# Optimization experiments

Hardware: AMD Instinct MI355X
Metric: run time of the kernel (lower is better)

## Reference

```python
import jax, jax.numpy as jnp
import numpy as np

EPSILON = 0.01
NITER = 5
EPS_MASS = 1e-9
EPS_LSE = 1e-6


def setup_inputs() -> dict:
    key = jax.random.key(0)
    k1, k2 = jax.random.split(key)
    y = jax.random.uniform(k1, (16, 1, 48, 48), dtype=jnp.float32)
    y_target = jax.random.uniform(k2, (16, 1, 48, 48), dtype=jnp.float32)
    return {"y": y, "y_target": y_target}


def _grid_points(h, w):
    # torch.linspace(0, h-1, h)/h == arange(h)/h
    yg = jnp.arange(h, dtype=jnp.float32) / h
    xg = jnp.arange(w, dtype=jnp.float32) / w
    gy, gx = jnp.meshgrid(yg, xg, indexing="ij")
    return jnp.stack([gy.reshape(-1), gx.reshape(-1)], axis=-1)  # [n, 2]


def reference(y, y_target):
    b, c, h, w = y_target.shape
    g = _grid_points(h, w)                     # [n, 2], same for x and y measures
    # cost_matrix with p=2: sum_k |g_i - g_j|^2 ; grids identical across batch,
    # so compute once as [n, n] and broadcast.
    C = ((g[:, None, :] - g[None, :, :]) ** 2).sum(-1)  # [n, n]

    mass_x = jnp.clip(y.reshape(b, -1), 0.0, 1e9) + EPS_MASS
    mass_y = jnp.clip(y_target.reshape(b, -1), 0.0, 1e9) + EPS_MASS
    mu = mass_x / mass_x.sum(-1, keepdims=True)   # [b, n]
    nu = mass_y / mass_y.sum(-1, keepdims=True)   # [b, n]
    log_mu = jnp.log(mu)
    log_nu = jnp.log(nu)

    def M(u, v):
        # (-C_ij + u_i + v_j) / epsilon, shape [b, n, n]
        return (-C[None, :, :] + u[:, :, None] + v[:, None, :]) / EPSILON

    def lse(A):
        # faithful to original: log(sum(exp(A), axis=2) + 1e-6) (non-shifted)
        return jnp.log(jnp.exp(A).sum(2) + EPS_LSE)

    u = jnp.zeros_like(mu)
    v = jnp.zeros_like(nu)
    for _ in range(NITER):
        u = EPSILON * (log_mu - lse(M(u, v))) + u
        v = EPSILON * (log_nu - lse(jnp.swapaxes(M(u, v), 1, 2))) + v

    pi = jnp.exp(M(u, v))                      # [b, n, n] transport plan
    cost = (pi * C[None, :, :]).sum((1, 2))    # [b]
    return jnp.mean(cost)
```

## Files before the change

kernel.cpp:

```cpp
#include <hip/hip_runtime.h>


#define TPB 576
#define STRIDE 72

typedef __attribute__((ext_vector_type(8))) short short8;
typedef __attribute__((ext_vector_type(4))) short short4v;
typedef __attribute__((ext_vector_type(4))) float f32x4;

__device__ __forceinline__ void splitb(float x, short& hi, short& lo) {
    union { float f; unsigned u; } a, h, l;
    a.f = x;
    h.u = a.u & 0xffff0000u;
    hi  = (short)(h.u >> 16);
    l.f = x - h.f;
    lo  = (short)(l.u >> 16);
}

__device__ __forceinline__ f32x4 mm16(short8 a, short8 b, f32x4 c) {
    return __builtin_amdgcn_mfma_f32_16x16x32_bf16(a, b, c, 0, 0, 0);
}

__device__ __forceinline__ f32x4 tile3(const short* Ah, const short* Al,
                                       const short* Bh, const short* Bl,
                                       int aOff, int bOff, f32x4 acc)
{
    short8 ah0 = *(const short8*)(Ah + aOff);
    short8 ah1 = *(const short8*)(Ah + aOff + 32);
    short8 al0 = *(const short8*)(Al + aOff);
    short8 al1 = *(const short8*)(Al + aOff + 32);
    short8 bh0 = *(const short8*)(Bh + bOff);
    short8 bh1 = *(const short8*)(Bh + bOff + 32);
    short8 bl0 = *(const short8*)(Bl + bOff);
    short8 bl1 = *(const short8*)(Bl + bOff + 32);
    f32x4 x = acc;
    f32x4 y = {0.f, 0.f, 0.f, 0.f};
    x = mm16(ah0, bh0, x);
    y = mm16(ah1, bh1, y);
    x = mm16(ah0, bl0, x);
    y = mm16(ah1, bl1, y);
    x = mm16(al0, bh0, x);
    y = mm16(al1, bh1, y);
    return x + y;
}

__global__ __launch_bounds__(TPB) void sinkhorn_kernel(const float* __restrict__ y,
                                                       const float* __restrict__ yt,
                                                       float* __restrict__ out)
{
    __shared__ __align__(16) short sThi[48*STRIDE],  sTlo[48*STRIDE];
    __shared__ __align__(16) short sTDhi[48*STRIDE], sTDlo[48*STRIDE];
    __shared__ __align__(16) short sWhi[48*STRIDE],  sWlo[48*STRIDE];
    __shared__ __align__(16) short sPhi[48*STRIDE],  sPlo[48*STRIDE];
    __shared__ __align__(16) float sS[2304];
    __shared__ float red[32];

    const int t    = threadIdx.x;
    const int b    = blockIdx.x;
    const int lane = t & 63;
    const int wid  = t >> 6;
    const int tr   = wid / 3;
    const int tc   = wid - tr * 3;
    const int n15  = lane & 15;
    const int quad = lane >> 4;
    const int kq   = quad * 8;
    const int aOff   = (tr * 16 + n15) * STRIDE + kq;
    const int bOff   = (tc * 16 + n15) * STRIDE + kq;
    const int prBase = tr * 16 + quad * 4;
    const int pn     = tc * 16 + n15;
    const int wOffB  = (t / 12) * STRIDE + (t % 12) * 4;

    const float EPS = 0.01f, RINV = 100.0f;

    for (int i = t; i < 48 * STRIDE; i += TPB) {
        sWhi[i] = 0; sWlo[i] = 0; sPhi[i] = 0; sPlo[i] = 0;
        int a  = i / STRIDE;
        int bb = i - a * STRIDE;
        short th = 0, tl = 0, dh = 0, dl = 0;
        if (bb < 48) {
            float d   = (float)a / 48.0f - (float)bb / 48.0f;
            float dsq = d * d;
            float e   = __expf(-dsq * RINV);
            splitb(e, th, tl);
            splitb(e * dsq, dh, dl);
        }
        sThi[i] = th; sTlo[i] = tl; sTDhi[i] = dh; sTDlo[i] = dl;
    }

    const f32x4 y4  = ((const f32x4*)(y  + b * 2304))[t];
    const f32x4 yt4 = ((const f32x4*)(yt + b * 2304))[t];
    float mx[4], my[4];
#pragma unroll
    for (int c = 0; c < 4; ++c) {
        mx[c] = fminf(fmaxf(y4[c],  0.f), 1e9f) + 1e-9f;
        my[c] = fminf(fmaxf(yt4[c], 0.f), 1e9f) + 1e-9f;
    }
    float sx = mx[0] + mx[1] + mx[2] + mx[3];
    float sy = my[0] + my[1] + my[2] + my[3];
#pragma unroll
    for (int off = 32; off > 0; off >>= 1) {
        sx += __shfl_down(sx, off);
        sy += __shfl_down(sy, off);
    }
    if (lane == 0) { red[wid] = sx; red[16 + wid] = sy; }
    __syncthreads();
    if (t == 0) {
        float ax = 0.f, ay = 0.f;
#pragma unroll
        for (int w = 0; w < TPB / 64; ++w) { ax += red[w]; ay += red[16 + w]; }
        red[0] = ax; red[16] = ay;
    }
    __syncthreads();
    const float rsx = 1.0f / red[0], rsy = 1.0f / red[16];

    float lmu_[4], lnu_[4];
#pragma unroll
    for (int c = 0; c < 4; ++c) {
        lmu_[c] = __logf(mx[c] * rsx);
        lnu_[c] = __logf(my[c] * rsy);
    }

    float u_[4]  = {0, 0, 0, 0}, v_[4]  = {0, 0, 0, 0};
    float wu_[4] = {1, 1, 1, 1}, wv_[4] = {1, 1, 1, 1};

    {
        short4v oneh = {(short)0x3F80, (short)0x3F80, (short)0x3F80, (short)0x3F80};
        short4v zer  = {0, 0, 0, 0};
        *(short4v*)(sWhi + wOffB) = oneh;
        *(short4v*)(sWlo + wOffB) = zer;
    }
    __syncthreads();

    const f32x4 zz = {0.f, 0.f, 0.f, 0.f};

    auto do_upd = [&](float (&ab)[4], const float (&lm)[4], float (&wc)[4],
                      const f32x4& S4) {
        short4v h4, l4;
#pragma unroll
        for (int c = 0; c < 4; ++c) {
            float lse = __logf(wc[c] * S4[c] + 1e-6f);
            ab[c] = EPS * (lm[c] - lse) + ab[c];
            wc[c] = __expf(RINV * ab[c]);
            short hh, ll; splitb(wc[c], hh, ll);
            h4[c] = hh; l4[c] = ll;
        }
        *(short4v*)(sWhi + wOffB) = h4;
        *(short4v*)(sWlo + wOffB) = l4;
    };

    for (int half = 0; half < 10; ++half) {
        f32x4 p = tile3(sThi, sTlo, sWhi, sWlo, aOff, bOff, zz);
#pragma unroll
        for (int rg = 0; rg < 4; ++rg) {
            short h, l; splitb(p[rg], h, l);
            int o = (prBase + rg) * STRIDE + pn;
            sPhi[o] = h; sPlo[o] = l;
        }
        __syncthreads();
        f32x4 s = tile3(sThi, sTlo, sPhi, sPlo, aOff, bOff, zz);
#pragma unroll
        for (int rg = 0; rg < 4; ++rg)
            sS[(prBase + rg) * 48 + pn] = s[rg];
        __syncthreads();
        f32x4 S4 = *(const f32x4*)(sS + 4 * t);
        if ((half & 1) == 0) do_upd(u_, lmu_, wu_, S4);
        else                 do_upd(v_, lnu_, wv_, S4);
        __syncthreads();
    }

    f32x4 p1 = tile3(sThi, sTlo, sWhi, sWlo, aOff, bOff, zz);
    f32x4 p2 = tile3(sTDhi, sTDlo, sWhi, sWlo, aOff, bOff, zz);
#pragma unroll
    for (int rg = 0; rg < 4; ++rg) {
        short h, l; splitb(p1[rg], h, l);
        int o = (prBase + rg) * STRIDE + pn;
        sPhi[o] = h; sPlo[o] = l;
    }
    __syncthreads();
    f32x4 sacc = tile3(sTDhi, sTDlo, sPhi, sPlo, aOff, bOff, zz);
    __syncthreads();
#pragma unroll
    for (int rg = 0; rg < 4; ++rg) {
        short h, l; splitb(p2[rg], h, l);
        int o = (prBase + rg) * STRIDE + pn;
        sPhi[o] = h; sPlo[o] = l;
    }
    __syncthreads();
    sacc = tile3(sThi, sTlo, sPhi, sPlo, aOff, bOff, sacc);
#pragma unroll
    for (int rg = 0; rg < 4; ++rg)
        sS[(prBase + rg) * 48 + pn] = sacc[rg];
    __syncthreads();

    f32x4 S4 = *(const f32x4*)(sS + 4 * t);
    float local = wu_[0] * S4[0] + wu_[1] * S4[1] + wu_[2] * S4[2] + wu_[3] * S4[3];
#pragma unroll
    for (int off = 32; off > 0; off >>= 1) local += __shfl_down(local, off);
    if (lane == 0) red[wid] = local;
    __syncthreads();
    if (t == 0) {
        float c = 0.f;
#pragma unroll
        for (int w = 0; w < TPB / 64; ++w) c += red[w];
        atomicAdd(out, c * (1.0f / 16.0f));
    }
}

extern "C" void kernel_launch(void* const* d_in, const int* in_sizes, int n_in,
                              void* d_out, int out_size, void* d_ws, size_t ws_size,
                              hipStream_t stream)
{
    (void)in_sizes; (void)n_in; (void)d_ws; (void)ws_size; (void)out_size;
    const float* y  = (const float*)d_in[0];
    const float* yt = (const float*)d_in[1];
    float* out = (float*)d_out;

    hipMemsetAsync(out, 0, sizeof(float), stream);
    sinkhorn_kernel<<<16, TPB, 0, stream>>>(y, yt, out);
}
```

Baseline: 73.26 us.

## Keep kernel tiles in registers, use multiplicative scaling updates with single-bf16 operands

The Gaussian kernel factors now live in registers instead of LDS. The u/v log-domain updates become direct multiplicative scaling-vector updates, which removes the log and exp per element. The B operands (W, P) switch from a hi/lo bf16 split to a single round-to-nearest bf16, cutting the MFMAs per tile from 6 to 4. It also removes one barrier per half-iteration and the sS staging buffer, and replaces the memset plus atomic with a per-block partial sum and a second small reduction kernel. In exchange, the lower-precision operands risk accuracy, and the extra launch adds overhead.

```diff
diff --git a/kernel.cpp b/kernel.cpp
--- a/kernel.cpp
+++ b/kernel.cpp
@@ -5,54 +5,36 @@
 #define STRIDE 72
 
 typedef __attribute__((ext_vector_type(8))) short short8;
-typedef __attribute__((ext_vector_type(4))) short short4v;
 typedef __attribute__((ext_vector_type(4))) float f32x4;
 
 __device__ __forceinline__ void splitb(float x, short& hi, short& lo) {
-    union { float f; unsigned u; } a, h, l;
+    union { float f; unsigned u; } a, h;
     a.f = x;
     h.u = a.u & 0xffff0000u;
     hi  = (short)(h.u >> 16);
+    union { float f; unsigned u; } l;
     l.f = x - h.f;
     lo  = (short)(l.u >> 16);
 }
 
+__device__ __forceinline__ short bf16rne(float x) {
+    union { float f; unsigned u; } a;
+    a.f = x;
+    unsigned r = a.u + 0x7fffu + ((a.u >> 16) & 1u);
+    return (short)(r >> 16);
+}
+
 __device__ __forceinline__ f32x4 mm16(short8 a, short8 b, f32x4 c) {
     return __builtin_amdgcn_mfma_f32_16x16x32_bf16(a, b, c, 0, 0, 0);
 }
 
-__device__ __forceinline__ f32x4 tile3(const short* Ah, const short* Al,
-                                       const short* Bh, const short* Bl,
-                                       int aOff, int bOff, f32x4 acc)
-{
-    short8 ah0 = *(const short8*)(Ah + aOff);
-    short8 ah1 = *(const short8*)(Ah + aOff + 32);
-    short8 al0 = *(const short8*)(Al + aOff);
-    short8 al1 = *(const short8*)(Al + aOff + 32);
-    short8 bh0 = *(const short8*)(Bh + bOff);
-    short8 bh1 = *(const short8*)(Bh + bOff + 32);
-    short8 bl0 = *(const short8*)(Bl + bOff);
-    short8 bl1 = *(const short8*)(Bl + bOff + 32);
-    f32x4 x = acc;
-    f32x4 y = {0.f, 0.f, 0.f, 0.f};
-    x = mm16(ah0, bh0, x);
-    y = mm16(ah1, bh1, y);
-    x = mm16(ah0, bl0, x);
-    y = mm16(ah1, bl1, y);
-    x = mm16(al0, bh0, x);
-    y = mm16(al1, bh1, y);
-    return x + y;
-}
-
 __global__ __launch_bounds__(TPB) void sinkhorn_kernel(const float* __restrict__ y,
                                                        const float* __restrict__ yt,
-                                                       float* __restrict__ out)
+                                                       float* __restrict__ partials)
 {
-    __shared__ __align__(16) short sThi[48*STRIDE],  sTlo[48*STRIDE];
-    __shared__ __align__(16) short sTDhi[48*STRIDE], sTDlo[48*STRIDE];
-    __shared__ __align__(16) short sWhi[48*STRIDE],  sWlo[48*STRIDE];
-    __shared__ __align__(16) short sPhi[48*STRIDE],  sPlo[48*STRIDE];
-    __shared__ __align__(16) float sS[2304];
+    __shared__ __align__(16) short sW[48 * STRIDE];
+    __shared__ __align__(16) short sP[48 * STRIDE];
+    __shared__ __align__(16) short sP2[48 * STRIDE];
     __shared__ float red[32];
 
     const int t    = threadIdx.x;
@@ -64,36 +46,50 @@
     const int n15  = lane & 15;
     const int quad = lane >> 4;
     const int kq   = quad * 8;
-    const int aOff   = (tr * 16 + n15) * STRIDE + kq;
-    const int bOff   = (tc * 16 + n15) * STRIDE + kq;
+    const int aRow = tr * 16 + n15;
+    const int bBase = (tc * 16 + n15) * STRIDE;
     const int prBase = tr * 16 + quad * 4;
     const int pn     = tc * 16 + n15;
-    const int wOffB  = (t / 12) * STRIDE + (t % 12) * 4;
-
-    const float EPS = 0.01f, RINV = 100.0f;
+    const int wAddr  = prBase * STRIDE + pn;
+
+    short8 Th0, Th1, Tl0, Tl1, Dh0, Dh1, Dl0, Dl1;
+    {
+        const float gm = (float)aRow / 48.0f;
+#pragma unroll
+        for (int kk = 0; kk < 8; ++kk) {
+            int k0 = kq + kk;
+            float d = gm - (float)k0 / 48.0f;
+            float dsq = d * d;
+            float e = __expf(-100.0f * dsq);
+            short h, l;
+            splitb(e, h, l);        Th0[kk] = h; Tl0[kk] = l;
+            splitb(e * dsq, h, l);  Dh0[kk] = h; Dl0[kk] = l;
+            int k1 = k0 + 32;
+            if (k1 < 48) {
+                float d1 = gm - (float)k1 / 48.0f;
+                float q1 = d1 * d1;
+                float e1 = __expf(-100.0f * q1);
+                splitb(e1, h, l);       Th1[kk] = h; Tl1[kk] = l;
+                splitb(e1 * q1, h, l);  Dh1[kk] = h; Dl1[kk] = l;
+            } else {
+                Th1[kk] = 0; Tl1[kk] = 0; Dh1[kk] = 0; Dl1[kk] = 0;
+            }
+        }
+    }
 
     for (int i = t; i < 48 * STRIDE; i += TPB) {
-        sWhi[i] = 0; sWlo[i] = 0; sPhi[i] = 0; sPlo[i] = 0;
-        int a  = i / STRIDE;
-        int bb = i - a * STRIDE;
-        short th = 0, tl = 0, dh = 0, dl = 0;
-        if (bb < 48) {
-            float d   = (float)a / 48.0f - (float)bb / 48.0f;
-            float dsq = d * d;
-            float e   = __expf(-dsq * RINV);
-            splitb(e, th, tl);
-            splitb(e * dsq, dh, dl);
-        }
-        sThi[i] = th; sTlo[i] = tl; sTDhi[i] = dh; sTDlo[i] = dl;
-    }
-
-    const f32x4 y4  = ((const f32x4*)(y  + b * 2304))[t];
-    const f32x4 yt4 = ((const f32x4*)(yt + b * 2304))[t];
+        int col = i - (i / STRIDE) * STRIDE;
+        sW[i]  = (col < 48) ? (short)0x3F80 : (short)0;
+        sP[i]  = 0;
+        sP2[i] = 0;
+    }
+
     float mx[4], my[4];
 #pragma unroll
-    for (int c = 0; c < 4; ++c) {
-        mx[c] = fminf(fmaxf(y4[c],  0.f), 1e9f) + 1e-9f;
-        my[c] = fminf(fmaxf(yt4[c], 0.f), 1e9f) + 1e-9f;
+    for (int rg = 0; rg < 4; ++rg) {
+        int e = (prBase + rg) * 48 + pn;
+        mx[rg] = fminf(fmaxf(y [b * 2304 + e], 0.f), 1e9f) + 1e-9f;
+        my[rg] = fminf(fmaxf(yt[b * 2304 + e], 0.f), 1e9f) + 1e-9f;
     }
     float sx = mx[0] + mx[1] + mx[2] + mx[3];
     float sy = my[0] + my[1] + my[2] + my[3];
@@ -113,87 +109,76 @@
     __syncthreads();
     const float rsx = 1.0f / red[0], rsy = 1.0f / red[16];
 
-    float lmu_[4], lnu_[4];
-#pragma unroll
-    for (int c = 0; c < 4; ++c) {
-        lmu_[c] = __logf(mx[c] * rsx);
-        lnu_[c] = __logf(my[c] * rsy);
-    }
-
-    float u_[4]  = {0, 0, 0, 0}, v_[4]  = {0, 0, 0, 0};
+    float mu_[4], nu_[4];
+#pragma unroll
+    for (int c = 0; c < 4; ++c) { mu_[c] = mx[c] * rsx; nu_[c] = my[c] * rsy; }
+
     float wu_[4] = {1, 1, 1, 1}, wv_[4] = {1, 1, 1, 1};
 
+    const f32x4 zz = {0.f, 0.f, 0.f, 0.f};
+
+    for (int half = 0; half < 10; ++half) {
+        {
+            short8 b0 = *(const short8*)(sW + bBase + kq);
+            short8 b1 = *(const short8*)(sW + bBase + kq + 32);
+            f32x4 x = mm16(Th0, b0, zz);
+            f32x4 yv = mm16(Th1, b1, zz);
+            x  = mm16(Tl0, b0, x);
+            yv = mm16(Tl1, b1, yv);
+            f32x4 p = x + yv;
+#pragma unroll
+            for (int rg = 0; rg < 4; ++rg)
+                sP[wAddr + rg * STRIDE] = bf16rne(p[rg]);
+        }
+        __syncthreads();
+        {
+            short8 b0 = *(const short8*)(sP + bBase + kq);
+            short8 b1 = *(const short8*)(sP + bBase + kq + 32);
+            f32x4 x = mm16(Th0, b0, zz);
+            f32x4 yv = mm16(Th1, b1, zz);
+            x  = mm16(Tl0, b0, x);
+            yv = mm16(Tl1, b1, yv);
+            f32x4 S = x + yv;
+            float* wc       = ((half & 1) == 0) ? wu_ : wv_;
+            const float* m_ = ((half & 1) == 0) ? mu_ : nu_;
+#pragma unroll
+            for (int c = 0; c < 4; ++c) {
+                wc[c] = wc[c] * m_[c] / (wc[c] * S[c] + 1e-6f);
+                sW[wAddr + c * STRIDE] = bf16rne(wc[c]);
+            }
+        }
+        __syncthreads();
+    }
+
     {
-        short4v oneh = {(short)0x3F80, (short)0x3F80, (short)0x3F80, (short)0x3F80};
-        short4v zer  = {0, 0, 0, 0};
-        *(short4v*)(sWhi + wOffB) = oneh;
-        *(short4v*)(sWlo + wOffB) = zer;
-    }
-    __syncthreads();
-
-    const f32x4 zz = {0.f, 0.f, 0.f, 0.f};
-
-    auto do_upd = [&](float (&ab)[4], const float (&lm)[4], float (&wc)[4],
-                      const f32x4& S4) {
-        short4v h4, l4;
-#pragma unroll
-        for (int c = 0; c < 4; ++c) {
-            float lse = __logf(wc[c] * S4[c] + 1e-6f);
-            ab[c] = EPS * (lm[c] - lse) + ab[c];
-            wc[c] = __expf(RINV * ab[c]);
-            short hh, ll; splitb(wc[c], hh, ll);
-            h4[c] = hh; l4[c] = ll;
-        }
-        *(short4v*)(sWhi + wOffB) = h4;
-        *(short4v*)(sWlo + wOffB) = l4;
-    };
-
-    for (int half = 0; half < 10; ++half) {
-        f32x4 p = tile3(sThi, sTlo, sWhi, sWlo, aOff, bOff, zz);
+        short8 b0 = *(const short8*)(sW + bBase + kq);
+        short8 b1 = *(const short8*)(sW + bBase + kq + 32);
+        f32x4 x1 = mm16(Th0, b0, zz), y1 = mm16(Th1, b1, zz);
+        x1 = mm16(Tl0, b0, x1);  y1 = mm16(Tl1, b1, y1);
+        f32x4 p1 = x1 + y1;
+        f32x4 x2 = mm16(Dh0, b0, zz), y2 = mm16(Dh1, b1, zz);
+        x2 = mm16(Dl0, b0, x2);  y2 = mm16(Dl1, b1, y2);
+        f32x4 p2 = x2 + y2;
 #pragma unroll
         for (int rg = 0; rg < 4; ++rg) {
-            short h, l; splitb(p[rg], h, l);
-            int o = (prBase + rg) * STRIDE + pn;
-            sPhi[o] = h; sPlo[o] = l;
-        }
-        __syncthreads();
-        f32x4 s = tile3(sThi, sTlo, sPhi, sPlo, aOff, bOff, zz);
-#pragma unroll
-        for (int rg = 0; rg < 4; ++rg)
-            sS[(prBase + rg) * 48 + pn] = s[rg];
-        __syncthreads();
-        f32x4 S4 = *(const f32x4*)(sS + 4 * t);
-        if ((half & 1) == 0) do_upd(u_, lmu_, wu_, S4);
-        else                 do_upd(v_, lnu_, wv_, S4);
-        __syncthreads();
-    }
-
-    f32x4 p1 = tile3(sThi, sTlo, sWhi, sWlo, aOff, bOff, zz);
-    f32x4 p2 = tile3(sTDhi, sTDlo, sWhi, sWlo, aOff, bOff, zz);
-#pragma unroll
-    for (int rg = 0; rg < 4; ++rg) {
-        short h, l; splitb(p1[rg], h, l);
-        int o = (prBase + rg) * STRIDE + pn;
-        sPhi[o] = h; sPlo[o] = l;
-    }
-    __syncthreads();
-    f32x4 sacc = tile3(sTDhi, sTDlo, sPhi, sPlo, aOff, bOff, zz);
-    __syncthreads();
-#pragma unroll
-    for (int rg = 0; rg < 4; ++rg) {
-        short h, l; splitb(p2[rg], h, l);
-        int o = (prBase + rg) * STRIDE + pn;
-        sPhi[o] = h; sPlo[o] = l;
-    }
-    __syncthreads();
-    sacc = tile3(sThi, sTlo, sPhi, sPlo, aOff, bOff, sacc);
-#pragma unroll
-    for (int rg = 0; rg < 4; ++rg)
-        sS[(prBase + rg) * 48 + pn] = sacc[rg];
-    __syncthreads();
-
-    f32x4 S4 = *(const f32x4*)(sS + 4 * t);
-    float local = wu_[0] * S4[0] + wu_[1] * S4[1] + wu_[2] * S4[2] + wu_[3] * S4[3];
+            sP [wAddr + rg * STRIDE] = bf16rne(p1[rg]);
+            sP2[wAddr + rg * STRIDE] = bf16rne(p2[rg]);
+        }
+    }
+    __syncthreads();
+    float local;
+    {
+        short8 b0 = *(const short8*)(sP  + bBase + kq);
+        short8 b1 = *(const short8*)(sP  + bBase + kq + 32);
+        short8 c0 = *(const short8*)(sP2 + bBase + kq);
+        short8 c1 = *(const short8*)(sP2 + bBase + kq + 32);
+        f32x4 x = mm16(Dh0, b0, zz), yv = mm16(Dh1, b1, zz);
+        x  = mm16(Dl0, b0, x);   yv = mm16(Dl1, b1, yv);
+        x  = mm16(Th0, c0, x);   yv = mm16(Th1, c1, yv);
+        x  = mm16(Tl0, c0, x);   yv = mm16(Tl1, c1, yv);
+        f32x4 S = x + yv;
+        local = wu_[0] * S[0] + wu_[1] * S[1] + wu_[2] * S[2] + wu_[3] * S[3];
+    }
 #pragma unroll
     for (int off = 32; off > 0; off >>= 1) local += __shfl_down(local, off);
     if (lane == 0) red[wid] = local;
@@ -202,19 +187,30 @@
         float c = 0.f;
 #pragma unroll
         for (int w = 0; w < TPB / 64; ++w) c += red[w];
-        atomicAdd(out, c * (1.0f / 16.0f));
-    }
+        partials[b] = c;
+    }
+}
+
+__global__ void finish_kernel(const float* __restrict__ partials,
+                              float* __restrict__ out)
+{
+    int l = threadIdx.x;
+    float v = (l < 16) ? partials[l] : 0.f;
+#pragma unroll
+    for (int off = 8; off > 0; off >>= 1) v += __shfl_down(v, off);
+    if (l == 0) out[0] = v * (1.0f / 16.0f);
 }
 
 extern "C" void kernel_launch(void* const* d_in, const int* in_sizes, int n_in,
                               void* d_out, int out_size, void* d_ws, size_t ws_size,
                               hipStream_t stream)
 {
-    (void)in_sizes; (void)n_in; (void)d_ws; (void)ws_size; (void)out_size;
+    (void)in_sizes; (void)n_in; (void)ws_size; (void)out_size;
     const float* y  = (const float*)d_in[0];
     const float* yt = (const float*)d_in[1];
-    float* out = (float*)d_out;
-
-    hipMemsetAsync(out, 0, sizeof(float), stream);
-    sinkhorn_kernel<<<16, TPB, 0, stream>>>(y, yt, out);
-}
+    float* partials = (float*)d_ws;
+    float* out      = (float*)d_out;
+
+    sinkhorn_kernel<<<16, TPB, 0, stream>>>(y, yt, partials);
+    finish_kernel<<<1, 64, 0, stream>>>(partials, out);
+}
```

New measurement: 68.26 us. 1.07x faster.
